# Performance work log

Measured on AMD Instinct MI355X. Metric: run time of the kernel, lower is better.

## Reference

```python
import jax, jax.numpy as jnp
import numpy as np

FLOAT_MIN = -1e20
L, B, H = 2048, 32, 1024


def setup_inputs() -> dict:
    key = jax.random.key(0)
    k0, k1, k2, k3, k4 = jax.random.split(key, 5)
    hidden = jax.random.normal(k0, (1, B, H), jnp.float32)
    encoder_outputs = jax.random.normal(k1, (L, B, H), jnp.float32)
    # nn.Linear(H, H) parameters for method='general'
    W = jax.random.normal(k2, (H, H), jnp.float32) / np.sqrt(H)
    b = jax.random.normal(k3, (H,), jnp.float32) * 0.01
    # lengths in [L//2, L] so every row has valid positions (original would NaN on length 0)
    lengths = jax.random.randint(k4, (B,), L // 2, L + 1, jnp.int32)
    return {"hidden": hidden, "encoder_outputs": encoder_outputs, "W": W, "b": b, "lengths": lengths}


def reference(hidden, encoder_outputs, W, b, lengths):
    # method='general': energy[b,i] = hidden[:,b] . (W @ enc[i,b] + bias)
    proj = jnp.einsum('lbh,gh->lbg', encoder_outputs, W) + b      # [L,B,H] Linear
    energies = jnp.einsum('lbg,bg->bl', proj, hidden[0])          # [B,L]
    pos = jnp.arange(L)[None, :]                                  # [1,L]
    valid = pos < lengths[:, None]                                # [B,L]
    energies = jnp.where(valid, energies, FLOAT_MIN)              # out-of-range stay FLOAT_MIN
    weights = jax.nn.softmax(energies, axis=-1)[:, None, :]       # [B,1,L]
    mask = valid[:, None, :].astype(weights.dtype)                # [B,1,L]
    masked = weights * mask
    sums = jnp.sum(masked, axis=-1, keepdims=True)                # renormalize over valid positions
    return masked / sums
```

## Files before the change

### kernel.cpp

```cpp
#include <hip/hip_runtime.h>

#define L_SEQ 2048
#define BATCH 32
#define HID   1024
#define FLOAT_MIN -1e20f

__global__ __launch_bounds__(256) void proj_kernel(
    const float* __restrict__ hidden,
    const float* __restrict__ W,
    const float* __restrict__ bias,
    float* __restrict__ v,
    float* __restrict__ c)
{
    __shared__ float  sh_hidden[HID];
    __shared__ float4 sh_part[8][32];
    __shared__ float  sh_red[4];

    const int b  = blockIdx.x >> 3;
    const int nt = blockIdx.x & 7;
    const int t  = threadIdx.x;

    ((float4*)sh_hidden)[t] = ((const float4*)(hidden + (size_t)b * HID))[t];
    __syncthreads();

    const int j4   = t & 31;
    const int half = t >> 5;
    const int n0   = nt * 128;

    float4 acc = make_float4(0.f, 0.f, 0.f, 0.f);
    const int kbase = half * 128;
    #pragma unroll 4
    for (int k = kbase; k < kbase + 128; ++k) {
        const float  hg = sh_hidden[k];
        const float4 w  = ((const float4*)(W + (size_t)k * HID + n0))[j4];
        acc.x += hg * w.x; acc.y += hg * w.y;
        acc.z += hg * w.z; acc.w += hg * w.w;
    }
    sh_part[half][j4] = acc;
    __syncthreads();

    if (t < 32) {
        float4 s = sh_part[0][t];
        #pragma unroll
        for (int h = 1; h < 8; ++h) {
            const float4 p = sh_part[h][t];
            s.x += p.x; s.y += p.y; s.z += p.z; s.w += p.w;
        }
        ((float4*)(v + (size_t)b * HID + n0))[t] = s;
    }

    if (nt == 0) {
        float p = 0.f;
        #pragma unroll
        for (int g = t; g < HID; g += 256) p += sh_hidden[g] * bias[g];
        #pragma unroll
        for (int off = 32; off > 0; off >>= 1) p += __shfl_down(p, off, 64);
        if ((t & 63) == 0) sh_red[t >> 6] = p;
        __syncthreads();
        if (t == 0) c[b] = sh_red[0] + sh_red[1] + sh_red[2] + sh_red[3];
    }
}

__global__ __launch_bounds__(256) void energy_kernel(
    const float* __restrict__ enc,
    const float* __restrict__ v,
    const float* __restrict__ c,
    float* __restrict__ energies)
{
    __shared__ float4 sv[256];

    const int b  = blockIdx.x >> 9;
    const int lt = blockIdx.x & 511;
    const int t  = threadIdx.x;

    sv[t] = ((const float4*)(v + (size_t)b * HID))[t];
    __syncthreads();

    const int wave = t >> 6;
    const int lane = t & 63;
    const int l    = lt * 4 + wave;

    const float4* ep = (const float4*)(enc + ((size_t)l * BATCH + b) * HID);
    float acc = 0.f;
    #pragma unroll
    for (int j = 0; j < 4; ++j) {
        const float4 e  = ep[j * 64 + lane];
        const float4 vv = sv[j * 64 + lane];
        acc += e.x * vv.x + e.y * vv.y + e.z * vv.z + e.w * vv.w;
    }
    #pragma unroll
    for (int off = 32; off > 0; off >>= 1) acc += __shfl_down(acc, off, 64);
    if (lane == 0) energies[(size_t)b * L_SEQ + l] = acc + c[b];
}

__global__ __launch_bounds__(256) void softmax_kernel(
    const float* __restrict__ energies,
    const int*   __restrict__ lengths,
    float* __restrict__ out)
{
    __shared__ float red[4];

    const int b   = blockIdx.x;
    const int t   = threadIdx.x;
    const int len = lengths[b];

    float e[8];
    float m = -INFINITY;
    #pragma unroll
    for (int i = 0; i < 8; ++i) {
        const int l = t + i * 256;
        e[i] = (l < len) ? energies[(size_t)b * L_SEQ + l] : FLOAT_MIN;
        m = fmaxf(m, e[i]);
    }
    #pragma unroll
    for (int off = 32; off > 0; off >>= 1) m = fmaxf(m, __shfl_down(m, off, 64));
    if ((t & 63) == 0) red[t >> 6] = m;
    __syncthreads();
    m = fmaxf(fmaxf(red[0], red[1]), fmaxf(red[2], red[3]));
    __syncthreads();

    float p[8];
    float s = 0.f;
    #pragma unroll
    for (int i = 0; i < 8; ++i) {
        p[i] = __expf(e[i] - m);
        s += p[i];
    }
    #pragma unroll
    for (int off = 32; off > 0; off >>= 1) s += __shfl_down(s, off, 64);
    if ((t & 63) == 0) red[t >> 6] = s;
    __syncthreads();
    s = red[0] + red[1] + red[2] + red[3];

    const float inv = 1.0f / s;
    #pragma unroll
    for (int i = 0; i < 8; ++i) {
        const int l = t + i * 256;
        out[(size_t)b * L_SEQ + l] = p[i] * inv;
    }
}

extern "C" void kernel_launch(void* const* d_in, const int* in_sizes, int n_in,
                              void* d_out, int out_size, void* d_ws, size_t ws_size,
                              hipStream_t stream) {
    const float* hidden  = (const float*)d_in[0];
    const float* enc     = (const float*)d_in[1];
    const float* W       = (const float*)d_in[2];
    const float* bias    = (const float*)d_in[3];
    const int*   lengths = (const int*)d_in[4];
    float* out = (float*)d_out;

    float* v        = (float*)d_ws;
    float* c        = v + BATCH * HID;
    float* energies = c + BATCH;

    proj_kernel   <<<256,                   256, 0, stream>>>(hidden, W, bias, v, c);
    energy_kernel <<<BATCH * (L_SEQ / 4),   256, 0, stream>>>(enc, v, c, energies);
    softmax_kernel<<<BATCH,                 256, 0, stream>>>(energies, lengths, out);
}
```

Before: 392.0 us.

## Skip encoder loads for masked positions and batch four rows per wave

The energy kernel now gives each wave four contiguous (l,b) rows of the encoder, walking memory linearly. It checks each row against lengths and skips loading masked rows, since those energies are overwritten by the softmax anyway. It reads v straight from global memory (cached) instead of staging it in shared memory, and issues all loads before any math to raise memory-level parallelism. This cuts HBM traffic by about a quarter on average, since lengths fall in [L/2, L], at the cost of more registers per thread.

```diff
diff --git a/kernel.cpp b/kernel.cpp
--- a/kernel.cpp
+++ b/kernel.cpp
@@ -65,32 +65,61 @@
     const float* __restrict__ enc,
     const float* __restrict__ v,
     const float* __restrict__ c,
+    const int*   __restrict__ lengths,
     float* __restrict__ energies)
 {
-    __shared__ float4 sv[256];
-
-    const int b  = blockIdx.x >> 9;
-    const int lt = blockIdx.x & 511;
-    const int t  = threadIdx.x;
-
-    sv[t] = ((const float4*)(v + (size_t)b * HID))[t];
-    __syncthreads();
-
+    const int t    = threadIdx.x;
     const int wave = t >> 6;
     const int lane = t & 63;
-    const int l    = lt * 4 + wave;
 
-    const float4* ep = (const float4*)(enc + ((size_t)l * BATCH + b) * HID);
-    float acc = 0.f;
+    const int rbase = blockIdx.x * 16 + wave;
+
+    int  r[4], b[4], l[4];
+    bool ok[4];
     #pragma unroll
-    for (int j = 0; j < 4; ++j) {
-        const float4 e  = ep[j * 64 + lane];
-        const float4 vv = sv[j * 64 + lane];
-        acc += e.x * vv.x + e.y * vv.y + e.z * vv.z + e.w * vv.w;
+    for (int i = 0; i < 4; ++i) {
+        r[i]  = rbase + 4 * i;
+        b[i]  = r[i] & (BATCH - 1);
+        l[i]  = r[i] >> 5;
+        ok[i] = l[i] < lengths[b[i]];
     }
+    if (!ok[0] && !ok[1] && !ok[2] && !ok[3]) return;
+
+    float4 e[4][4];
     #pragma unroll
-    for (int off = 32; off > 0; off >>= 1) acc += __shfl_down(acc, off, 64);
-    if (lane == 0) energies[(size_t)b * L_SEQ + l] = acc + c[b];
+    for (int i = 0; i < 4; ++i) {
+        if (ok[i]) {
+            const float4* ep = (const float4*)(enc + (size_t)r[i] * HID);
+            #pragma unroll
+            for (int j = 0; j < 4; ++j) e[i][j] = ep[j * 64 + lane];
+        }
+    }
+
+    float acc[4] = {0.f, 0.f, 0.f, 0.f};
+    #pragma unroll
+    for (int i = 0; i < 4; ++i) {
+        if (ok[i]) {
+            const float4* vp = (const float4*)(v + (size_t)b[i] * HID);
+            #pragma unroll
+            for (int j = 0; j < 4; ++j) {
+                const float4 vv = vp[j * 64 + lane];
+                const float4 ee = e[i][j];
+                acc[i] += ee.x * vv.x + ee.y * vv.y + ee.z * vv.z + ee.w * vv.w;
+            }
+        }
+    }
+
+    #pragma unroll
+    for (int off = 32; off > 0; off >>= 1) {
+        #pragma unroll
+        for (int i = 0; i < 4; ++i) acc[i] += __shfl_down(acc[i], off, 64);
+    }
+
+    if (lane == 0) {
+        #pragma unroll
+        for (int i = 0; i < 4; ++i)
+            if (ok[i]) energies[(size_t)b[i] * L_SEQ + l[i]] = acc[i] + c[b[i]];
+    }
 }
 
 __global__ __launch_bounds__(256) void softmax_kernel(
@@ -154,7 +183,7 @@
     float* c        = v + BATCH * HID;
     float* energies = c + BATCH;
 
-    proj_kernel   <<<256,                   256, 0, stream>>>(hidden, W, bias, v, c);
-    energy_kernel <<<BATCH * (L_SEQ / 4),   256, 0, stream>>>(enc, v, c, energies);
-    softmax_kernel<<<BATCH,                 256, 0, stream>>>(energies, lengths, out);
+    proj_kernel   <<<256,                  256, 0, stream>>>(hidden, W, bias, v, c);
+    energy_kernel <<<(L_SEQ * BATCH) / 16, 256, 0, stream>>>(enc, v, c, lengths, energies);
+    softmax_kernel<<<BATCH,                256, 0, stream>>>(energies, lengths, out);
 }
```

After: 369.8 us. 5.7% less time.
